# Optimization experiments

Hardware: AMD Instinct MI355X
Metric: run time of the kernel (lower is better)

## Reference

```python
import jax, jax.numpy as jnp
import numpy as np

N_NODES = 50000
N_EDGES = 800000
D_IN = 128
D_OUT = 64


def setup_inputs() -> dict:
    key = jax.random.key(0)
    k1, k2, k3, k4 = jax.random.split(key, 4)
    x = jax.random.normal(k1, (N_NODES, D_IN), dtype=jnp.float32)
    W = jax.random.normal(k2, (D_OUT, D_IN), dtype=jnp.float32) * (1.0 / np.sqrt(D_IN))
    b = jnp.zeros((D_OUT,), dtype=jnp.float32)
    row = jax.random.randint(k3, (N_EDGES,), 0, N_NODES, dtype=jnp.int32)
    col = jax.random.randint(k4, (N_EDGES,), 0, N_NODES, dtype=jnp.int32)
    return {"x": x, "W": W, "b": b, "row": row, "col": col}


def reference(x, W, b, row, col):
    # Linear projection: [N, D_in] -> [N, D_out]
    h = x @ W.T + b
    n = x.shape[0]
    # Row-normalized SpMM: out[i] = (1/deg(i)) * sum_{(i,j) in E} h[j]
    msg = h[col]  # gather source features: [E, D_out]
    summed = jax.ops.segment_sum(msg, row, num_segments=n)
    deg = jax.ops.segment_sum(jnp.ones_like(row, dtype=h.dtype), row, num_segments=n)
    out = summed / jnp.maximum(deg, 1.0)[:, None]
    return out
```

## Files before the change

### kernel.cpp

```cpp
#include <hip/hip_runtime.h>
#include <hip/hip_bf16.h>

#define D_IN   128
#define D_OUT  64
#define CAP    32
#define MAX_USHORT_NODES 65536
#define BIN_SHIFT 8
#define MAX_BINS  256
#define BIN_CAP   8192
#define P1_BLOCKS 256
#define P2_THREADS 512

using frag_ab = __attribute__((ext_vector_type(8))) short;
using frag_cd = __attribute__((ext_vector_type(4))) float;

static __device__ __forceinline__ short f2bf(float f) {
    union { float f; unsigned u; } v; v.f = f;
    unsigned r = v.u + 0x7FFFu + ((v.u >> 16) & 1u);
    return (short)(r >> 16);
}
static __device__ __forceinline__ float bf1(unsigned short s) {
    union { unsigned u; float f; } v; v.u = ((unsigned)s) << 16; return v.f;
}

__global__ void prep_kernel(const float* __restrict__ x,
                            const float* __restrict__ W,
                            const float* __restrict__ bvec,
                            unsigned short* __restrict__ h,
                            const int* __restrict__ row,
                            const int* __restrict__ col,
                            unsigned* __restrict__ scratch,
                            int* __restrict__ cursor,
                            int* __restrict__ ovfA_cnt,
                            unsigned* __restrict__ ovfA_list,
                            int ovfA_cap, int n_nodes, int n_edges,
                            int n_bins, int proj_blocks) {
    __shared__ int hist[MAX_BINS];
    __shared__ int base[MAX_BINS];

    if ((int)blockIdx.x >= proj_blocks) {
        const int bid = (int)blockIdx.x - proj_blocks;
        const int per = (n_edges + P1_BLOCKS - 1) / P1_BLOCKS;
        const int e0 = bid * per;
        const int e1 = min(e0 + per, n_edges);

        for (int i = threadIdx.x; i < n_bins; i += 256) hist[i] = 0;
        __syncthreads();
        for (int e = e0 + (int)threadIdx.x; e < e1; e += 256)
            atomicAdd(&hist[row[e] >> BIN_SHIFT], 1);
        __syncthreads();
        for (int i = threadIdx.x; i < n_bins; i += 256) {
            const int hcnt = hist[i];
            base[i] = hcnt > 0 ? atomicAdd(&cursor[i * 16], hcnt) : 0;
            hist[i] = 0;
        }
        __syncthreads();
        for (int e = e0 + (int)threadIdx.x; e < e1; e += 256) {
            const int r = row[e];
            const int c = col[e];
            const int bn = r >> BIN_SHIFT;
            const int loc = atomicAdd(&hist[bn], 1);
            const int off = base[bn] + loc;
            if (off < BIN_CAP) {
                scratch[(size_t)bn * BIN_CAP + off] =
                    (unsigned)(r & 255) | ((unsigned)c << 8);
            } else {
                const int k = atomicAdd(ovfA_cnt, 1);
                if (k < ovfA_cap) ovfA_list[k] = (unsigned)r | ((unsigned)c << 16);
            }
        }
        return;
    }

    const int lane = (int)threadIdx.x & 63;
    const int wid  = (int)((blockIdx.x * 256 + threadIdx.x) >> 6);
    const int nwaves = proj_blocks * 4;
    const int m    = lane & 15;
    const int quad = lane >> 4;

    frag_ab Bf[4][4];
#pragma unroll
    for (int kk = 0; kk < 4; ++kk) {
#pragma unroll
        for (int nt = 0; nt < 4; ++nt) {
            const float* wp = W + (size_t)(nt * 16 + m) * D_IN + kk * 32 + quad * 8;
            const float4 w0 = *(const float4*)wp;
            const float4 w1 = *(const float4*)(wp + 4);
            frag_ab f;
            f[0] = f2bf(w0.x); f[1] = f2bf(w0.y); f[2] = f2bf(w0.z); f[3] = f2bf(w0.w);
            f[4] = f2bf(w1.x); f[5] = f2bf(w1.y); f[6] = f2bf(w1.z); f[7] = f2bf(w1.w);
            Bf[kk][nt] = f;
        }
    }
    float bb[4];
#pragma unroll
    for (int nt = 0; nt < 4; ++nt) bb[nt] = bvec[nt * 16 + m];

    const int ntiles = (n_nodes + 15) / 16;
    for (int tile = wid; tile < ntiles; tile += nwaves) {
        const int node_base = tile * 16;
        int arow = node_base + m;
        if (arow > n_nodes - 1) arow = n_nodes - 1;

        float4 xv[8];
        const float* xr = x + (size_t)arow * D_IN + quad * 8;
#pragma unroll
        for (int kk = 0; kk < 4; ++kk) {
            xv[2 * kk]     = *(const float4*)(xr + kk * 32);
            xv[2 * kk + 1] = *(const float4*)(xr + kk * 32 + 4);
        }

        frag_cd acc[4];
#pragma unroll
        for (int nt = 0; nt < 4; ++nt) {
            acc[nt][0] = bb[nt]; acc[nt][1] = bb[nt];
            acc[nt][2] = bb[nt]; acc[nt][3] = bb[nt];
        }
#pragma unroll
        for (int kk = 0; kk < 4; ++kk) {
            const float4 x0 = xv[2 * kk], x1 = xv[2 * kk + 1];
            frag_ab A;
            A[0] = f2bf(x0.x); A[1] = f2bf(x0.y); A[2] = f2bf(x0.z); A[3] = f2bf(x0.w);
            A[4] = f2bf(x1.x); A[5] = f2bf(x1.y); A[6] = f2bf(x1.z); A[7] = f2bf(x1.w);
#pragma unroll
            for (int nt = 0; nt < 4; ++nt)
                acc[nt] = __builtin_amdgcn_mfma_f32_16x16x32_bf16(A, Bf[kk][nt],
                                                                  acc[nt], 0, 0, 0);
        }
#pragma unroll
        for (int nt = 0; nt < 4; ++nt) {
#pragma unroll
            for (int r = 0; r < 4; ++r) {
                const int node = node_base + quad * 4 + r;
                if (node < n_nodes)
                    h[(size_t)node * D_OUT + nt * 16 + m] =
                        (unsigned short)f2bf(acc[nt][r]);
            }
        }
    }
}

__global__ __launch_bounds__(P2_THREADS)
void binpass2_kernel(const unsigned* __restrict__ scratch,
                     const int* __restrict__ cursor,
                     int* __restrict__ deg, unsigned short* __restrict__ bucket,
                     int* __restrict__ ovfB_cnt, unsigned* __restrict__ ovfB_list,
                     int ovfB_cap,
                     const int* __restrict__ ovfA_cnt,
                     const unsigned* __restrict__ ovfA_list, int ovfA_cap,
                     int n_nodes) {
    __shared__ int ldeg[256];
    __shared__ unsigned short lbuck[256 * CAP];
    const int bin = (int)blockIdx.x;
    const int node0 = bin << BIN_SHIFT;
    const int nrows = min(256, n_nodes - node0);
    int cnt = cursor[bin * 16]; if (cnt > BIN_CAP) cnt = BIN_CAP;

    if (bin == 0) {
        int cA = *ovfA_cnt; if (cA > ovfA_cap) cA = ovfA_cap;
        for (int k = threadIdx.x; k < cA; k += P2_THREADS)
            atomicAdd(&deg[ovfA_list[k] & 0xFFFFu], 1);
    }

    for (int i = threadIdx.x; i < 256; i += P2_THREADS) ldeg[i] = 0;
    __syncthreads();
    for (int i = threadIdx.x; i < cnt; i += P2_THREADS) {
        const unsigned rec = scratch[(size_t)bin * BIN_CAP + i];
        const int rl = rec & 255;
        const int c  = (int)(rec >> 8);
        const int s = atomicAdd(&ldeg[rl], 1);
        if (s < CAP) {
            lbuck[(rl << 5) + s] = (unsigned short)c;
        } else {
            const int k = atomicAdd(ovfB_cnt, 1);
            if (k < ovfB_cap)
                ovfB_list[k] = (unsigned)(node0 + rl) | ((unsigned)c << 16);
        }
    }
    __syncthreads();
    for (int i = threadIdx.x; i < nrows; i += P2_THREADS)
        atomicAdd(&deg[node0 + i], ldeg[i]);
    uint4* dst = (uint4*)(bucket + (size_t)node0 * CAP);
    const uint4* src = (const uint4*)lbuck;
    const int nu4 = nrows * (CAP / 8);
    for (int i = threadIdx.x; i < nu4; i += P2_THREADS) dst[i] = src[i];
}

__global__ __launch_bounds__(256)
void gather3_kernel(const unsigned short* __restrict__ h16,
                    const int* __restrict__ deg,
                    const unsigned short* __restrict__ bucket,
                    const int* __restrict__ ovf_cnts,
                    const unsigned* __restrict__ ovfA_list,
                    const unsigned* __restrict__ ovfB_list,
                    int ovf_cap,
                    float* __restrict__ out, int n_nodes) {
    const int lane = (int)threadIdx.x & 63;
    const int wv = (int)((blockIdx.x * blockDim.x + threadIdx.x) >> 6);
    if (wv >= n_nodes) return;
    const int node = __builtin_amdgcn_readfirstlane(wv);

    const int d = deg[node];
    const int dc = d < CAP ? d : CAP;
    const unsigned* brow = (const unsigned*)(bucket + (size_t)node * CAP);
    unsigned rec[CAP / 2];
#pragma unroll
    for (int i = 0; i < CAP / 2; ++i) rec[i] = brow[i];

    float acc = 0.f;
#pragma unroll
    for (int k = 0; k < 16; ++k) {
        const unsigned idx = (k & 1) ? (rec[k >> 1] >> 16)
                                     : (rec[k >> 1] & 0xFFFFu);
        const unsigned use = (k < dc) ? idx : 0u;
        const float v = bf1(h16[(size_t)use * D_OUT + lane]);
        acc += (k < dc) ? v : 0.f;
    }
    if (dc > 16) {
#pragma unroll
        for (int k = 16; k < 32; ++k) {
            const unsigned idx = (k & 1) ? (rec[k >> 1] >> 16)
                                         : (rec[k >> 1] & 0xFFFFu);
            const unsigned use = (k < dc) ? idx : 0u;
            const float v = bf1(h16[(size_t)use * D_OUT + lane]);
            acc += (k < dc) ? v : 0.f;
        }
    }

    int cA = ovf_cnts[0]; if (cA > ovf_cap) cA = ovf_cap;
    int cB = ovf_cnts[1]; if (cB > ovf_cap) cB = ovf_cap;
    if (cA + cB > 0) {
        for (int k = 0; k < cA; ++k) {
            const unsigned r2 = ovfA_list[k];
            if ((int)(r2 & 0xFFFFu) == node)
                acc += bf1(h16[(size_t)(r2 >> 16) * D_OUT + lane]);
        }
        for (int k = 0; k < cB; ++k) {
            const unsigned r2 = ovfB_list[k];
            if ((int)(r2 & 0xFFFFu) == node)
                acc += bf1(h16[(size_t)(r2 >> 16) * D_OUT + lane]);
        }
    }

    out[(size_t)node * D_OUT + lane] = acc * (1.0f / fmaxf((float)d, 1.0f));
}

__global__ void proj_only_kernel(const float* __restrict__ x,
                                 const float* __restrict__ W,
                                 const float* __restrict__ bvec,
                                 float* __restrict__ h, int n_nodes) {
    const int lane = (int)threadIdx.x & 63;
    const int wave = (int)((blockIdx.x * blockDim.x + threadIdx.x) >> 6);
    const int nwaves = (int)((gridDim.x * blockDim.x) >> 6);
    const float bias = bvec[lane];
    for (int node = wave; node < n_nodes; node += nwaves) {
        const float* xr = &x[(size_t)node * D_IN];
        float acc = bias;
#pragma unroll
        for (int k = 0; k < D_IN; ++k) acc += xr[k] * W[lane * D_IN + k];
        h[(size_t)node * D_OUT + lane] = acc;
    }
}

__global__ void scatter_kernel(const float* __restrict__ h,
                               const int* __restrict__ row,
                               const int* __restrict__ col,
                               float* __restrict__ out,
                               int* __restrict__ deg,
                               long long n_tasks) {
    long long t = (long long)blockIdx.x * blockDim.x + threadIdx.x;
    const long long stride = (long long)gridDim.x * blockDim.x;
    for (; t < n_tasks; t += stride) {
        const int e = (int)(t >> 6);
        const int c = (int)(t & 63);
        atomicAdd(&out[(size_t)row[e] * D_OUT + c], h[(size_t)col[e] * D_OUT + c]);
        if (c == 0) atomicAdd(&deg[row[e]], 1);
    }
}

__global__ void div_kernel(float* __restrict__ out,
                           const int* __restrict__ deg, int n_total) {
    int t = blockIdx.x * blockDim.x + threadIdx.x;
    if (t < n_total) {
        out[t] *= 1.0f / fmaxf((float)deg[t >> 6], 1.0f);
    }
}

extern "C" void kernel_launch(void* const* d_in, const int* in_sizes, int n_in,
                              void* d_out, int out_size, void* d_ws, size_t ws_size,
                              hipStream_t stream) {
    const float* x   = (const float*)d_in[0];
    const float* W   = (const float*)d_in[1];
    const float* b   = (const float*)d_in[2];
    const int*   row = (const int*)d_in[3];
    const int*   col = (const int*)d_in[4];
    float* out = (float*)d_out;

    const int n_nodes = in_sizes[0] / D_IN;
    const int n_edges = in_sizes[3];
    const int n_bins  = (n_nodes + 255) >> BIN_SHIFT;

    char* p = (char*)d_ws;
    unsigned short* h = (unsigned short*)p;
    p += (size_t)n_nodes * D_OUT * sizeof(unsigned short);
    int* deg = (int*)p;            p += (size_t)n_nodes * sizeof(int);
    int* ovf_cnts = (int*)p;       p += 256;
    int* cursor = (int*)p;         p += (size_t)MAX_BINS * 16 * sizeof(int);
    unsigned* ovfA_list = (unsigned*)p;  p += (size_t)n_edges * sizeof(unsigned);
    unsigned* ovfB_list = (unsigned*)p;  p += (size_t)n_edges * sizeof(unsigned);
    unsigned short* bucket = (unsigned short*)p;
    p += (size_t)n_nodes * CAP * sizeof(unsigned short);
    unsigned* scratch = (unsigned*)p;
    p += (size_t)n_bins * BIN_CAP * sizeof(unsigned);
    const size_t needed = (size_t)(p - (char*)d_ws);

    if (ws_size >= needed && n_nodes <= MAX_USHORT_NODES) {
        hipMemsetAsync(deg, 0,
                       (size_t)n_nodes * sizeof(int) + 256 +
                       (size_t)MAX_BINS * 16 * sizeof(int), stream);

        const int ntiles = (n_nodes + 15) / 16;
        const int proj_blocks = (ntiles + 3) / 4;
        prep_kernel<<<proj_blocks + P1_BLOCKS, 256, 0, stream>>>(
            x, W, b, h, row, col, scratch, cursor, &ovf_cnts[0], ovfA_list,
            n_edges, n_nodes, n_edges, n_bins, proj_blocks);

        binpass2_kernel<<<n_bins, P2_THREADS, 0, stream>>>(
            scratch, cursor, deg, bucket, &ovf_cnts[1], ovfB_list, n_edges,
            &ovf_cnts[0], ovfA_list, n_edges, n_nodes);

        const int grid = (n_nodes + 3) / 4;
        gather3_kernel<<<grid, 256, 0, stream>>>(
            h, deg, bucket, ovf_cnts, ovfA_list, ovfB_list, n_edges,
            out, n_nodes);
    } else {
        float* hf = (float*)d_ws;
        int* degf = (int*)((char*)d_ws + (size_t)n_nodes * D_OUT * sizeof(float));
        hipMemsetAsync(out, 0, (size_t)out_size * sizeof(float), stream);
        hipMemsetAsync(degf, 0, (size_t)n_nodes * sizeof(int), stream);
        proj_only_kernel<<<1024, 256, 0, stream>>>(x, W, b, hf, n_nodes);
        const long long n_tasks = (long long)n_edges * D_OUT;
        scatter_kernel<<<16384, 256, 0, stream>>>(hf, row, col, out, degf, n_tasks);
        const int n_total = n_nodes * D_OUT;
        div_kernel<<<(n_total + 255) / 256, 256, 0, stream>>>(out, degf, n_total);
    }
}
```

Before: 138.5 us.

## Locally sort edge chunks by bin in LDS before coalesced scatter to scratch

```diff
diff --git a/kernel.cpp b/kernel.cpp
--- a/kernel.cpp
+++ b/kernel.cpp
@@ -8,7 +8,7 @@
 #define BIN_SHIFT 8
 #define MAX_BINS  256
 #define BIN_CAP   8192
-#define P1_BLOCKS 256
+#define P1_EDGES  2048
 #define P2_THREADS 512
 
 using frag_ab = __attribute__((ext_vector_type(8))) short;
@@ -34,39 +34,58 @@
                             int* __restrict__ ovfA_cnt,
                             unsigned* __restrict__ ovfA_list,
                             int ovfA_cap, int n_nodes, int n_edges,
-                            int n_bins, int proj_blocks) {
+                            int proj_blocks) {
     __shared__ int hist[MAX_BINS];
-    __shared__ int base[MAX_BINS];
+    __shared__ int segs[MAX_BINS];
+    __shared__ int lofs[MAX_BINS];
+    __shared__ int gbase[MAX_BINS];
+    __shared__ unsigned sorted[P1_EDGES];
 
     if ((int)blockIdx.x >= proj_blocks) {
         const int bid = (int)blockIdx.x - proj_blocks;
-        const int per = (n_edges + P1_BLOCKS - 1) / P1_BLOCKS;
-        const int e0 = bid * per;
-        const int e1 = min(e0 + per, n_edges);
-
-        for (int i = threadIdx.x; i < n_bins; i += 256) hist[i] = 0;
-        __syncthreads();
-        for (int e = e0 + (int)threadIdx.x; e < e1; e += 256)
+        const int e0 = bid * P1_EDGES;
+        const int e1 = min(e0 + P1_EDGES, n_edges);
+        const int cnt = e1 - e0;
+        const int i = (int)threadIdx.x;
+
+        hist[i] = 0;
+        __syncthreads();
+        for (int e = e0 + i; e < e1; e += 256)
             atomicAdd(&hist[row[e] >> BIN_SHIFT], 1);
         __syncthreads();
-        for (int i = threadIdx.x; i < n_bins; i += 256) {
-            const int hcnt = hist[i];
-            base[i] = hcnt > 0 ? atomicAdd(&cursor[i * 16], hcnt) : 0;
-            hist[i] = 0;
-        }
-        __syncthreads();
-        for (int e = e0 + (int)threadIdx.x; e < e1; e += 256) {
+        segs[i] = hist[i];
+        __syncthreads();
+        for (int s = 1; s < MAX_BINS; s <<= 1) {
+            int v = segs[i];
+            if (i >= s) v += segs[i - s];
+            __syncthreads();
+            segs[i] = v;
+            __syncthreads();
+        }
+        {
+            const int hc = hist[i];
+            const int ex = segs[i] - hc;
+            lofs[i] = ex;
+            hist[i] = ex;
+            gbase[i] = hc > 0 ? atomicAdd(&cursor[i * 16], hc) : 0;
+        }
+        __syncthreads();
+        for (int e = e0 + i; e < e1; e += 256) {
             const int r = row[e];
-            const int c = col[e];
-            const int bn = r >> BIN_SHIFT;
-            const int loc = atomicAdd(&hist[bn], 1);
-            const int off = base[bn] + loc;
+            const unsigned rec = (unsigned)r | ((unsigned)col[e] << 16);
+            const int pos = atomicAdd(&lofs[r >> BIN_SHIFT], 1);
+            sorted[pos] = rec;
+        }
+        __syncthreads();
+        for (int k = i; k < cnt; k += 256) {
+            const unsigned rec = sorted[k];
+            const int bn = (int)(rec & 0xFFFFu) >> BIN_SHIFT;
+            const int off = gbase[bn] + (k - hist[bn]);
             if (off < BIN_CAP) {
-                scratch[(size_t)bn * BIN_CAP + off] =
-                    (unsigned)(r & 255) | ((unsigned)c << 8);
+                scratch[(size_t)bn * BIN_CAP + off] = rec;
             } else {
-                const int k = atomicAdd(ovfA_cnt, 1);
-                if (k < ovfA_cap) ovfA_list[k] = (unsigned)r | ((unsigned)c << 16);
+                const int t = atomicAdd(ovfA_cnt, 1);
+                if (t < ovfA_cap) ovfA_list[t] = rec;
             }
         }
         return;
@@ -167,7 +186,7 @@
     for (int i = threadIdx.x; i < cnt; i += P2_THREADS) {
         const unsigned rec = scratch[(size_t)bin * BIN_CAP + i];
         const int rl = rec & 255;
-        const int c  = (int)(rec >> 8);
+        const int c  = (int)(rec >> 16);
         const int s = atomicAdd(&ldeg[rl], 1);
         if (s < CAP) {
             lbuck[(rl << 5) + s] = (unsigned short)c;
@@ -321,9 +340,10 @@
 
         const int ntiles = (n_nodes + 15) / 16;
         const int proj_blocks = (ntiles + 3) / 4;
-        prep_kernel<<<proj_blocks + P1_BLOCKS, 256, 0, stream>>>(
+        const int p1_blocks = (n_edges + P1_EDGES - 1) / P1_EDGES;
+        prep_kernel<<<proj_blocks + p1_blocks, 256, 0, stream>>>(
             x, W, b, h, row, col, scratch, cursor, &ovf_cnts[0], ovfA_list,
-            n_edges, n_nodes, n_edges, n_bins, proj_blocks);
+            n_edges, n_nodes, n_edges, proj_blocks);
 
         binpass2_kernel<<<n_bins, P2_THREADS, 0, stream>>>(
             scratch, cursor, deg, bucket, &ovf_cnts[1], ovfB_list, n_edges,
```

Result: faster. 135.3 us (-2.3%).
